# Kernel optimization log

Measured on AMD Instinct MI355X. Metric: run time of the kernel, lower is better.

The kernel has to match this reference:

```python
import jax, jax.numpy as jnp
import numpy as np
import math


def _layernorm(x, g, b, eps=1e-5):
    m = x.mean(-1, keepdims=True)
    v = x.var(-1, keepdims=True)
    return (x - m) / jnp.sqrt(v + eps) * g + b


def _ssd(log_decay, frequency, b_r, b_i, chunk):
    # SSD eigenstate evolution: chunk-local complex decay-mask matmuls + sequential inter-chunk state scan
    B, T, K = b_r.shape
    T_pad = -(-T // chunk) * chunk
    if T_pad > T:
        pad = T_pad - T
        b_r = jnp.pad(b_r, ((0, 0), (0, pad), (0, 0)))
        b_i = jnp.pad(b_i, ((0, 0), (0, pad), (0, 0)))
    n_chunks = T_pad // chunk
    mag = jax.nn.sigmoid(log_decay)                      # (K,)
    pos = jnp.arange(chunk, dtype=b_r.dtype)             # (C,)
    mag_pow = mag[None, :] ** pos[:, None]               # (C,K)
    phases = pos[:, None] * frequency[None, :]           # (C,K)
    kernel_r = mag_pow * jnp.cos(phases)
    kernel_i = mag_pow * jnp.sin(phases)
    diffs = pos[None, :] - pos[:, None]                  # (C,C), faithful to torch: pos.unsqueeze(0)-pos.unsqueeze(1)
    mask = (diffs >= 0).astype(b_r.dtype)[:, :, None]
    idx = jnp.clip(diffs, 0, None).astype(jnp.int32)
    L_r = kernel_r[idx] * mask                           # (C,C,K)
    L_i = kernel_i[idx] * mask
    Br = b_r.reshape(B, n_chunks, chunk, K)
    Bi = b_i.reshape(B, n_chunks, chunk, K)
    # intra-chunk complex contraction
    intra_r = jnp.einsum('ijk,bnjk->bnik', L_r, Br) - jnp.einsum('ijk,bnjk->bnik', L_i, Bi)
    intra_i = jnp.einsum('ijk,bnjk->bnik', L_r, Bi) + jnp.einsum('ijk,bnjk->bnik', L_i, Br)
    prop_r = L_r[:, 0, :]                                # (C,K)
    prop_i = L_i[:, 0, :]

    def step(carry, chunk_in):
        sr, si = carry                                   # (B,K)
        ir, ii = chunk_in                                # (B,C,K)
        corr_r = prop_r[None] * sr[:, None] - prop_i[None] * si[:, None]
        corr_i = prop_r[None] * si[:, None] + prop_i[None] * sr[:, None]
        out_r = ir + corr_r
        out_i = ii + corr_i
        return (out_r[:, -1], out_i[:, -1]), (out_r, out_i)

    init = (jnp.zeros((B, K), b_r.dtype), jnp.zeros((B, K), b_r.dtype))
    _, (o_r, o_i) = jax.lax.scan(step, init, (intra_r.transpose(1, 0, 2, 3), intra_i.transpose(1, 0, 2, 3)))
    c_r = o_r.transpose(1, 0, 2, 3).reshape(B, T_pad, K)[:, :T]
    c_i = o_i.transpose(1, 0, 2, 3).reshape(B, T_pad, K)[:, :T]
    return c_r, c_i


def setup_inputs() -> dict:
    B, T, D, K, H, CONV = 4, 4096, 1024, 64, 4, 4
    Kh = K // H
    mlp = 4 * D
    ks = jax.random.split(jax.random.key(0), 12)

    def n(k, shape, s):
        return (jax.random.normal(k, shape) * s).astype(jnp.float32)

    return {
        'x': n(ks[0], (B, T, D), 1.0),
        'in_proj_w': n(ks[1], (2 * K, D), 1.0 / math.sqrt(D)),
        'conv_w': n(ks[2], (2 * K, 1, CONV), 0.5),
        'conv_b': jnp.zeros((2 * K,), jnp.float32),
        'log_decay': jax.random.uniform(ks[3], (K,), minval=-3.0, maxval=-1.5).astype(jnp.float32),
        'frequency': jnp.linspace(0.0, 2 * math.pi * (1 - 1.0 / K), K).astype(jnp.float32),
        'coupling': (jnp.eye(Kh)[None] + 0.01 * jax.random.normal(ks[4], (H, Kh, Kh)) / math.sqrt(Kh)).astype(jnp.float32),
        'out_proj_w': n(ks[5], (D, 2 * K), 1.0 / math.sqrt(2 * K)),
        'gate_w': n(ks[6], (D, D), 1.0 / math.sqrt(D)),
        'gate_b': jnp.full((D,), -2.0, jnp.float32),
        'mlp_w1': n(ks[7], (mlp, D), 1.0 / math.sqrt(D)),
        'mlp_b1': jnp.zeros((mlp,), jnp.float32),
        'mlp_w2': n(ks[8], (D, mlp), 1.0 / math.sqrt(mlp)),
        'mlp_b2': jnp.zeros((D,), jnp.float32),
        'ln1_g': jnp.ones((D,), jnp.float32), 'ln1_b': jnp.zeros((D,), jnp.float32),
        'ln2_g': jnp.ones((D,), jnp.float32), 'ln2_b': jnp.zeros((D,), jnp.float32),
    }


def reference(x, in_proj_w, conv_w, conv_b, log_decay, frequency, coupling,
              out_proj_w, gate_w, gate_b, mlp_w1, mlp_b1, mlp_w2, mlp_b2,
              ln1_g, ln1_b, ln2_g, ln2_b):
    B, T, D = x.shape
    K2 = in_proj_w.shape[0]
    K = K2 // 2
    CHUNK = 64
    H, Kh = coupling.shape[0], coupling.shape[1]
    residual = x
    xn = _layernorm(x, ln1_g, ln1_b)
    beta = xn @ in_proj_w.T                              # (B,T,2K)
    kconv = conv_w.shape[-1]
    # causal depthwise conv1d (torch pads both sides then truncates to T == left-pad kconv-1)
    bc = jax.lax.conv_general_dilated(
        beta.transpose(0, 2, 1), conv_w, (1,), [(kconv - 1, 0)],
        feature_group_count=K2, dimension_numbers=('NCH', 'OIH', 'NCH'))
    beta = jax.nn.silu((bc + conv_b[None, :, None]).transpose(0, 2, 1))
    beta_r, beta_i = beta[..., :K], beta[..., K:]
    c_r, c_i = _ssd(log_decay, frequency, beta_r, beta_i, CHUNK)
    c_r = jnp.einsum('hjk,bthk->bthj', coupling, c_r.reshape(B, T, H, Kh)).reshape(B, T, K)
    c_i = jnp.einsum('hjk,bthk->bthj', coupling, c_i.reshape(B, T, H, Kh)).reshape(B, T, K)
    eig = jnp.concatenate([c_r, c_i], axis=-1)           # (B,T,2K)
    h = eig @ out_proj_w.T
    gate = jax.nn.sigmoid(xn @ gate_w.T + gate_b)
    x1 = residual + gate * h
    xn2 = _layernorm(x1, ln2_g, ln2_b)
    out = x1 + (jax.nn.silu(xn2 @ mlp_w1.T + mlp_b1) @ mlp_w2.T + mlp_b2)
    return out, eig
```

## Files before the change

kernel.cpp:

```cpp
#include <hip/hip_runtime.h>
#include <hip/hip_bf16.h>


#define FIR_LAG 20

typedef __attribute__((ext_vector_type(8))) short    bf16x8;
typedef __attribute__((ext_vector_type(4))) float    f32x4;
typedef __attribute__((ext_vector_type(4))) unsigned short ushort4_t;

__device__ __forceinline__ unsigned short f2bf(float f) {
    union { __hip_bfloat16 b; unsigned short u; } cv;
    cv.b = __float2bfloat16(f);
    return cv.u;
}
__device__ __forceinline__ float bf2f(unsigned short u) {
    return __uint_as_float((unsigned)u << 16);
}

__device__ __forceinline__ void gload_lds16(const unsigned short* g, unsigned short* l) {
    __builtin_amdgcn_global_load_lds(
        (const __attribute__((address_space(1))) unsigned int*)g,
        (__attribute__((address_space(3))) unsigned int*)l, 16, 0, 0);
}

__global__ __launch_bounds__(256) void cvt_bf16_kernel(
    const float* __restrict__ in, unsigned short* __restrict__ out, int n)
{
    int i = (blockIdx.x * 256 + threadIdx.x) * 8;
    if (i >= n) return;
    float4 a = *(const float4*)(in + i);
    float4 b = *(const float4*)(in + i + 4);
    ushort4_t o0 = { f2bf(a.x), f2bf(a.y), f2bf(a.z), f2bf(a.w) };
    ushort4_t o1 = { f2bf(b.x), f2bf(b.y), f2bf(b.z), f2bf(b.w) };
    *(ushort4_t*)(out + i)     = o0;
    *(ushort4_t*)(out + i + 4) = o1;
}

__global__ __launch_bounds__(256) void ln_kernel(
    const float* __restrict__ in, const float* __restrict__ g,
    const float* __restrict__ b, unsigned short* __restrict__ out)
{
    const size_t row = blockIdx.x;
    const int t = threadIdx.x;
    float4 v = ((const float4*)(in + row * 1024))[t];
    float s  = v.x + v.y + v.z + v.w;
    float s2 = v.x*v.x + v.y*v.y + v.z*v.z + v.w*v.w;
    #pragma unroll
    for (int o = 32; o > 0; o >>= 1) {
        s  += __shfl_down(s, o);
        s2 += __shfl_down(s2, o);
    }
    __shared__ float red[8];
    __shared__ float mv[2];
    const int wv = t >> 6;
    if ((t & 63) == 0) { red[wv] = s; red[4 + wv] = s2; }
    __syncthreads();
    if (t == 0) {
        float a  = red[0] + red[1] + red[2] + red[3];
        float a2 = red[4] + red[5] + red[6] + red[7];
        float mean = a * (1.f / 1024.f);
        float var  = a2 * (1.f / 1024.f) - mean * mean;
        mv[0] = mean;
        mv[1] = rsqrtf(var + 1e-5f);
    }
    __syncthreads();
    const float mean = mv[0], rstd = mv[1];
    float4 gg = ((const float4*)g)[t];
    float4 bb = ((const float4*)b)[t];
    ushort4_t o4 = { f2bf((v.x - mean) * rstd * gg.x + bb.x),
                     f2bf((v.y - mean) * rstd * gg.y + bb.y),
                     f2bf((v.z - mean) * rstd * gg.z + bb.z),
                     f2bf((v.w - mean) * rstd * gg.w + bb.w) };
    *(ushort4_t*)(out + row * 1024 + t * 4) = o4;
}

__global__ __launch_bounds__(256) void conv_silu_kernel(
    const float* __restrict__ bp, const float* __restrict__ cw,
    const float* __restrict__ cb, float* __restrict__ beta, int T)
{
    const int idx = blockIdx.x * 256 + threadIdx.x;
    const int c  = idx & 127;
    const int bt = idx >> 7;
    const int t  = bt & (T - 1);
    float acc = cb[c];
    #pragma unroll
    for (int j = 0; j < 4; ++j) {
        int ts = t - 3 + j;
        if (ts >= 0) acc += cw[c * 4 + j] * bp[(size_t)(bt - 3 + j) * 128 + c];
    }
    beta[(size_t)bt * 128 + c] = acc / (1.f + expf(-acc));
}

__global__ __launch_bounds__(256) void fir_coupling_kernel(
    const float* __restrict__ beta, const float* __restrict__ log_decay,
    const float* __restrict__ freq, const float* __restrict__ coup,
    float* __restrict__ eig, unsigned short* __restrict__ eig_bf, int T)
{
    __shared__ float sb[65][128];
    const int blk = blockIdx.x;
    const int nch = T >> 6;
    const int b = blk / nch;
    const int n = blk - b * nch;
    const size_t base = ((size_t)b * T + (size_t)n * 64) * 128;
    const int tid = threadIdx.x;

    #pragma unroll
    for (int it = 0; it < 8; ++it) {
        int f = tid + it * 256;
        int r = f >> 5, c4 = f & 31;
        *(float4*)&sb[1 + r][c4 * 4] =
            *(const float4*)(beta + base + (size_t)r * 128 + c4 * 4);
    }
    if (tid < 32) {
        float4 z = make_float4(0.f, 0.f, 0.f, 0.f);
        *(float4*)&sb[0][tid * 4] =
            (n > 0) ? *(const float4*)(beta + base - 128 + tid * 4) : z;
    }
    __syncthreads();

    const int k  = tid & 63;
    const int tq = tid >> 6;
    const float mag = 1.f / (1.f + expf(-log_decay[k]));
    const float w = freq[k];
    const float rr = mag * cosf(w), ri = mag * sinf(w);
    float cr[16], ci[16];
    #pragma unroll
    for (int m = 0; m < 16; ++m) { cr[m] = 0.f; ci[m] = 0.f; }
    float zr = 1.f, zi = 0.f;
    for (int e = 0; e <= FIR_LAG; ++e) {
        #pragma unroll
        for (int m = 0; m < 16; ++m) {
            int i = tq * 16 + m;
            int src = i + e;
            if (src <= 63) {
                float br = sb[1 + src][k];
                float bi = sb[1 + src][64 + k];
                cr[m] += zr * br - zi * bi;
                ci[m] += zr * bi + zi * br;
            }
        }
        float nzr = zr * rr - zi * ri;
        zi = zr * ri + zi * rr;
        zr = nzr;
    }
    if (tq == 0) {
        cr[0] += sb[0][k];
        ci[0] += sb[0][64 + k];
    }
    __syncthreads();
    #pragma unroll
    for (int m = 0; m < 16; ++m) {
        int i = tq * 16 + m;
        sb[i][k] = cr[m];
        sb[i][64 + k] = ci[m];
    }
    __syncthreads();
    const int h = k >> 4, j = k & 15;
    float cp[16];
    #pragma unroll
    for (int q = 0; q < 16; ++q) cp[q] = coup[(h * 16 + j) * 16 + q];
    #pragma unroll
    for (int m = 0; m < 16; ++m) {
        int i = tq * 16 + m;
        float sr = 0.f, si = 0.f;
        #pragma unroll
        for (int q = 0; q < 16; ++q) {
            sr += cp[q] * sb[i][h * 16 + q];
            si += cp[q] * sb[i][64 + h * 16 + q];
        }
        size_t o = base + (size_t)i * 128;
        eig[o + k]         = sr;
        eig[o + 64 + k]    = si;
        eig_bf[o + k]      = f2bf(sr);
        eig_bf[o + 64 + k] = f2bf(si);
    }
}

__global__ __launch_bounds__(256) void gemm_mfma_f32out(
    const unsigned short* __restrict__ A, const unsigned short* __restrict__ B,
    float* __restrict__ C, int M, int N, int K)
{
    constexpr int BM = 128, BK = 32;
    __shared__ unsigned short As[BM * BK];
    __shared__ unsigned short Bs[BM * BK];
    const int tid  = threadIdx.x;
    const int lane = tid & 63;
    const int wave = tid >> 6;
    const int wm = wave >> 1, wn = wave & 1;
    const int bm = blockIdx.y * BM;
    const int bn = blockIdx.x * BM;

    f32x4 acc[4][4];
    #pragma unroll
    for (int m = 0; m < 4; ++m)
        #pragma unroll
        for (int n = 0; n < 4; ++n) acc[m][n] = (f32x4){0.f, 0.f, 0.f, 0.f};

    const int frow = lane & 15;
    const int fk   = (lane >> 4) * 8;
    const int srow = tid >> 2;
    const int sc   = (tid & 3) * 8;

    for (int k0 = 0; k0 < K; k0 += BK) {
        #pragma unroll
        for (int it = 0; it < 2; ++it) {
            int row = it * 64 + srow;
            int ci  = it * 256 + tid;
            gload_lds16(A + (size_t)(bm + row) * K + k0 + sc, As + ci * 8);
            gload_lds16(B + (size_t)(bn + row) * K + k0 + sc, Bs + ci * 8);
        }
        __syncthreads();
        bf16x8 af[4], bfr[4];
        #pragma unroll
        for (int m = 0; m < 4; ++m)
            af[m] = *(const bf16x8*)(As + (wm * 64 + m * 16 + frow) * BK + fk);
        #pragma unroll
        for (int n = 0; n < 4; ++n)
            bfr[n] = *(const bf16x8*)(Bs + (wn * 64 + n * 16 + frow) * BK + fk);
        #pragma unroll
        for (int m = 0; m < 4; ++m)
            #pragma unroll
            for (int n = 0; n < 4; ++n)
                acc[m][n] = __builtin_amdgcn_mfma_f32_16x16x32_bf16(
                    af[m], bfr[n], acc[m][n], 0, 0, 0);
        __syncthreads();
    }

    const int r0 = (lane >> 4) * 4;
    const int cc = lane & 15;
    #pragma unroll
    for (int m = 0; m < 4; ++m)
        #pragma unroll
        for (int n = 0; n < 4; ++n) {
            const int col = bn + wn * 64 + n * 16 + cc;
            #pragma unroll
            for (int j = 0; j < 4; ++j) {
                const int row = bm + wm * 64 + m * 16 + r0 + j;
                C[(size_t)row * N + col] = acc[m][n][j];
            }
        }
}

template<int EPI, typename OT>
__global__ __launch_bounds__(512) void gemm256(
    const unsigned short* __restrict__ A, const unsigned short* __restrict__ B,
    OT* __restrict__ C, int M, int N, int K,
    const float* __restrict__ bias,
    const float* __restrict__ p1, const unsigned short* __restrict__ p2)
{
    constexpr int BM = 256, BN = 256;
    __shared__ unsigned short Asw[4 * 256 * 32];
    __shared__ unsigned short Bsw[4 * 256 * 32];
    const int tid  = threadIdx.x;
    const int lane = tid & 63;
    const int wave = tid >> 6;
    const int wm = wave >> 2;
    const int wn = wave & 3;

    const int nbn = N / BN;
    const int nwg = gridDim.x;
    int orig = blockIdx.x;
    int xcd = orig & 7, ixc = orig >> 3;
    int q = nwg >> 3, r = nwg & 7;
    int wgid = (xcd < r ? xcd * (q + 1) : r * (q + 1) + (xcd - r) * q) + ixc;
    const int bm = (wgid / nbn) * BM;
    const int bn = (wgid % nbn) * BN;

    f32x4 acc[8][4];
    #pragma unroll
    for (int m = 0; m < 8; ++m)
        #pragma unroll
        for (int n = 0; n < 4; ++n) acc[m][n] = (f32x4){0.f, 0.f, 0.f, 0.f};

    const int frow   = lane & 15;
    const int lk     = lane >> 4;
    const int achunk = lk ^ (frow & 3);

    const unsigned short* Abase = A + (size_t)bm * K;
    const unsigned short* Bbase = B + (size_t)bn * K;

#define STAGE_H(G, DS, KH)                                                   \
    {                                                                        \
        _Pragma("unroll")                                                    \
        for (int s = 0; s < 2; ++s) {                                        \
            int cid = s * 512 + tid;                                         \
            int row = cid >> 2, c = cid & 3;                                 \
            int gch = c ^ (row & 3);                                         \
            gload_lds16((G) + (size_t)row * K + (KH) * 32 + gch * 8,         \
                        (DS) + ((KH) & 3) * 8192 + cid * 8);                 \
        }                                                                    \
    }

#define LDA(MH, KH)                                                          \
    _Pragma("unroll")                                                        \
    for (int m = 0; m < 4; ++m) {                                            \
        int row = wm * 128 + (MH) * 64 + m * 16 + frow;                      \
        af[m] = *(const bf16x8*)(Asw + ((KH) & 3) * 8192 + row * 32 +        \
                                 achunk * 8);                                \
    }

#define LDB(KH)                                                              \
    _Pragma("unroll")                                                        \
    for (int n = 0; n < 4; ++n) {                                            \
        int row = wn * 64 + n * 16 + frow;                                   \
        bfv[n] = *(const bf16x8*)(Bsw + ((KH) & 3) * 8192 + row * 32 +       \
                                  achunk * 8);                               \
    }

#define BARRIER                                                              \
    asm volatile("s_barrier" ::: "memory");                                  \
    __builtin_amdgcn_sched_barrier(0);

#define MFMA_PH(MH)                                                          \
    asm volatile("s_waitcnt lgkmcnt(0)" ::: "memory");                       \
    __builtin_amdgcn_sched_barrier(0);                                       \
    __builtin_amdgcn_s_setprio(1);                                           \
    _Pragma("unroll")                                                        \
    for (int m = 0; m < 4; ++m)                                              \
        _Pragma("unroll")                                                    \
        for (int n = 0; n < 4; ++n)                                          \
            acc[(MH) * 4 + m][n] = __builtin_amdgcn_mfma_f32_16x16x32_bf16(  \
                af[m], bfv[n], acc[(MH) * 4 + m][n], 0, 0, 0);               \
    __builtin_amdgcn_s_setprio(0);

    const int NKH = K >> 5;

    STAGE_H(Abase, Asw, 0)
    STAGE_H(Bbase, Bsw, 0)
    STAGE_H(Abase, Asw, 1)
    STAGE_H(Bbase, Bsw, 1)
    STAGE_H(Abase, Asw, 2)
    STAGE_H(Bbase, Bsw, 2)
    asm volatile("s_waitcnt vmcnt(8)" ::: "memory");
    BARRIER

    for (int kh = 0; kh < NKH; ++kh) {
        bf16x8 af[4], bfv[4];
        LDA(0, kh)
        LDB(kh)
        if (kh + 3 < NKH) { STAGE_H(Abase, Asw, kh + 3) }
        BARRIER
        MFMA_PH(0)
        BARRIER
        LDA(1, kh)
        if (kh + 3 < NKH) { STAGE_H(Bbase, Bsw, kh + 3) }
        {
            int rem = NKH - 1 - kh;
            if (rem >= 3) {
                asm volatile("s_waitcnt vmcnt(8)" ::: "memory");
            } else if (rem == 2) {
                asm volatile("s_waitcnt vmcnt(4)" ::: "memory");
            } else if (rem == 1) {
                asm volatile("s_waitcnt vmcnt(0)" ::: "memory");
            }
        }
        BARRIER
        MFMA_PH(1)
        BARRIER
    }
#undef STAGE_H
#undef LDA
#undef LDB
#undef BARRIER
#undef MFMA_PH

    const int r0 = (lane >> 4) * 4;
    const int cc = lane & 15;
    #pragma unroll
    for (int m = 0; m < 8; ++m) {
        #pragma unroll
        for (int n = 0; n < 4; ++n) {
            const int col = bn + wn * 64 + n * 16 + cc;
            #pragma unroll
            for (int j = 0; j < 4; ++j) {
                const int row = bm + wm * 128 + m * 16 + r0 + j;
                const size_t idx = (size_t)row * N + col;
                const float v = acc[m][n][j];
                if constexpr (EPI == 0) {
                    C[idx] = v;
                } else if constexpr (EPI == 1) {
                    float pre = v + bias[col];
                    float gt = 1.f / (1.f + expf(-pre));
                    C[idx] = p1[idx] + gt * bf2f(p2[idx]);
                } else if constexpr (EPI == 2) {
                    float pre = v + bias[col];
                    C[idx] = (OT)__float2bfloat16(pre / (1.f + expf(-pre)));
                } else if constexpr (EPI == 3) {
                    C[idx] = p1[idx] + v + bias[col];
                } else {
                    C[idx] = (OT)__float2bfloat16(v);
                }
            }
        }
    }
}

extern "C" void kernel_launch(void* const* d_in, const int* in_sizes, int n_in,
                              void* d_out, int out_size, void* d_ws, size_t ws_size,
                              hipStream_t stream)
{
    const float* x        = (const float*)d_in[0];
    const float* in_proj  = (const float*)d_in[1];
    const float* conv_w   = (const float*)d_in[2];
    const float* conv_b   = (const float*)d_in[3];
    const float* log_dec  = (const float*)d_in[4];
    const float* freq     = (const float*)d_in[5];
    const float* coup     = (const float*)d_in[6];
    const float* out_proj = (const float*)d_in[7];
    const float* gate_w   = (const float*)d_in[8];
    const float* gate_b   = (const float*)d_in[9];
    const float* mlp_w1   = (const float*)d_in[10];
    const float* mlp_b1   = (const float*)d_in[11];
    const float* mlp_w2   = (const float*)d_in[12];
    const float* mlp_b2   = (const float*)d_in[13];
    const float* ln1_g    = (const float*)d_in[14];
    const float* ln1_b    = (const float*)d_in[15];
    const float* ln2_g    = (const float*)d_in[16];
    const float* ln2_b    = (const float*)d_in[17];

    const int B = 4, T = 4096, D = 1024;
    const int M = B * T;

    float* out = (float*)d_out;
    float* eig = out + (size_t)M * D;
    float* bpre = eig;

    char* w = (char*)d_ws;
    unsigned short* xn_bf = (unsigned short*)w; w += (size_t)M * 1024 * 2;
    float* x1             = (float*)w;          w += (size_t)M * 1024 * 4;
    float* beta           = (float*)w;          w += (size_t)M * 128 * 4;
    unsigned short* mid   = (unsigned short*)w; w += (size_t)M * 4096 * 2;
    unsigned short* eig_bf= (unsigned short*)w; w += (size_t)M * 128 * 2;
    unsigned short* wb_inproj = (unsigned short*)w; w += (size_t)128 * 1024 * 2;
    unsigned short* wb_outproj= (unsigned short*)w; w += (size_t)1024 * 128 * 2;
    unsigned short* wb_gate   = (unsigned short*)w; w += (size_t)1024 * 1024 * 2;
    unsigned short* wb_mlp1   = (unsigned short*)w; w += (size_t)4096 * 1024 * 2;
    unsigned short* wb_mlp2   = (unsigned short*)w; w += (size_t)1024 * 4096 * 2;
    unsigned short* h_bf = mid;

    cvt_bf16_kernel<<<(128 * 1024) / 2048, 256, 0, stream>>>(in_proj, wb_inproj, 128 * 1024);
    cvt_bf16_kernel<<<(1024 * 128) / 2048, 256, 0, stream>>>(out_proj, wb_outproj, 1024 * 128);
    cvt_bf16_kernel<<<(1024 * 1024) / 2048, 256, 0, stream>>>(gate_w, wb_gate, 1024 * 1024);
    cvt_bf16_kernel<<<(4096 * 1024) / 2048, 256, 0, stream>>>(mlp_w1, wb_mlp1, 4096 * 1024);
    cvt_bf16_kernel<<<(1024 * 4096) / 2048, 256, 0, stream>>>(mlp_w2, wb_mlp2, 1024 * 4096);

    ln_kernel<<<M, 256, 0, stream>>>(x, ln1_g, ln1_b, xn_bf);
    gemm_mfma_f32out<<<dim3(1, M / 128), 256, 0, stream>>>(
        xn_bf, wb_inproj, bpre, M, 128, 1024);
    conv_silu_kernel<<<(M * 128) / 256, 256, 0, stream>>>(bpre, conv_w, conv_b, beta, T);
    fir_coupling_kernel<<<B * (T / 64), 256, 0, stream>>>(
        beta, log_dec, freq, coup, eig, eig_bf, T);
    gemm256<4, __hip_bfloat16><<<(M / 256) * (1024 / 256), 512, 0, stream>>>(
        eig_bf, wb_outproj, (__hip_bfloat16*)h_bf, M, 1024, 128,
        nullptr, nullptr, nullptr);
    gemm256<1, float><<<(M / 256) * (1024 / 256), 512, 0, stream>>>(
        xn_bf, wb_gate, x1, M, 1024, 1024, gate_b, x, h_bf);
    ln_kernel<<<M, 256, 0, stream>>>(x1, ln2_g, ln2_b, xn_bf);
    gemm256<2, __hip_bfloat16><<<(M / 256) * (4096 / 256), 512, 0, stream>>>(
        xn_bf, wb_mlp1, (__hip_bfloat16*)mid, M, 4096, 1024, mlp_b1, nullptr, nullptr);
    gemm256<3, float><<<(M / 256) * (1024 / 256), 512, 0, stream>>>(
        mid, wb_mlp2, out, M, 1024, 4096, mlp_b2, x1, nullptr);
}
```

Before: 563.5 us.

## Double-buffer BK=64 tiles with 8-chunk XOR swizzle in gemm256

Replaces the four-slot ring of 32-wide K half-tiles (prefetched three ahead) with two buffers of 64-wide K tiles, each split into two 32-wide halves. It also adopts a row-pair layout whose 8 chunks are XOR-swizzled by row pair. The aim is to cut LDS bank conflicts and the number of vmcnt waits and barriers per unit of K. The trade-off is a shallower prefetch distance, which may expose more global-load latency.

```diff
diff --git a/kernel.cpp b/kernel.cpp
--- a/kernel.cpp
+++ b/kernel.cpp
@@ -248,9 +248,9 @@
     const float* __restrict__ bias,
     const float* __restrict__ p1, const unsigned short* __restrict__ p2)
 {
-    constexpr int BM = 256, BN = 256;
-    __shared__ unsigned short Asw[4 * 256 * 32];
-    __shared__ unsigned short Bsw[4 * 256 * 32];
+    constexpr int BM = 256, BN = 256, BK = 64;
+    __shared__ unsigned short As[2 * 2 * 8192];
+    __shared__ unsigned short Bs[2 * 2 * 8192];
     const int tid  = threadIdx.x;
     const int lane = tid & 63;
     const int wave = tid >> 6;
@@ -272,46 +272,47 @@
         #pragma unroll
         for (int n = 0; n < 4; ++n) acc[m][n] = (f32x4){0.f, 0.f, 0.f, 0.f};
 
-    const int frow   = lane & 15;
-    const int lk     = lane >> 4;
-    const int achunk = lk ^ (frow & 3);
+    const int frow = lane & 15;
+    const int lk   = lane >> 4;
 
     const unsigned short* Abase = A + (size_t)bm * K;
     const unsigned short* Bbase = B + (size_t)bn * K;
 
-#define STAGE_H(G, DS, KH)                                                   \
+#define STAGE(G, LB, NBUF, KH, K0)                                           \
     {                                                                        \
         _Pragma("unroll")                                                    \
         for (int s = 0; s < 2; ++s) {                                        \
             int cid = s * 512 + tid;                                         \
-            int row = cid >> 2, c = cid & 3;                                 \
-            int gch = c ^ (row & 3);                                         \
-            gload_lds16((G) + (size_t)row * K + (KH) * 32 + gch * 8,         \
-                        (DS) + ((KH) & 3) * 8192 + cid * 8);                 \
+            int rp  = cid >> 3, cp = cid & 7;                                \
+            int c   = cp ^ (rp & 7);                                         \
+            int g   = 2 * rp + (c >> 2);                                     \
+            gload_lds16((G) + (size_t)g * K + (K0) + (KH) * 32 + (c & 3) * 8,\
+                        (LB) + ((NBUF) * 2 + (KH)) * 8192 + cid * 8);        \
         }                                                                    \
     }
 
-#define LDA(MH, KH)                                                          \
+#define LDA(MH, KH, BUF)                                                     \
     _Pragma("unroll")                                                        \
     for (int m = 0; m < 4; ++m) {                                            \
-        int row = wm * 128 + (MH) * 64 + m * 16 + frow;                      \
-        af[m] = *(const bf16x8*)(Asw + ((KH) & 3) * 8192 + row * 32 +        \
-                                 achunk * 8);                                \
-    }
-
-#define LDB(KH)                                                              \
+        int R  = wm * 128 + (MH) * 64 + m * 16 + frow;                       \
+        int rp = R >> 1;                                                     \
+        int ch = (((R & 1) << 2) | lk) ^ (rp & 7);                           \
+        af[m] = *(const bf16x8*)(As + ((BUF) * 2 + (KH)) * 8192 +            \
+                                 rp * 64 + ch * 8);                          \
+    }
+
+#define LDB(KH, BUF)                                                         \
     _Pragma("unroll")                                                        \
     for (int n = 0; n < 4; ++n) {                                            \
-        int row = wn * 64 + n * 16 + frow;                                   \
-        bfv[n] = *(const bf16x8*)(Bsw + ((KH) & 3) * 8192 + row * 32 +       \
-                                  achunk * 8);                               \
-    }
-
-#define BARRIER                                                              \
+        int R  = wn * 64 + n * 16 + frow;                                    \
+        int rp = R >> 1;                                                     \
+        int ch = (((R & 1) << 2) | lk) ^ (rp & 7);                           \
+        bfv[n] = *(const bf16x8*)(Bs + ((BUF) * 2 + (KH)) * 8192 +           \
+                                  rp * 64 + ch * 8);                         \
+    }
+
+#define PH_TAIL(MH)                                                          \
     asm volatile("s_barrier" ::: "memory");                                  \
-    __builtin_amdgcn_sched_barrier(0);
-
-#define MFMA_PH(MH)                                                          \
     asm volatile("s_waitcnt lgkmcnt(0)" ::: "memory");                       \
     __builtin_amdgcn_sched_barrier(0);                                       \
     __builtin_amdgcn_s_setprio(1);                                           \
@@ -321,48 +322,48 @@
         for (int n = 0; n < 4; ++n)                                          \
             acc[(MH) * 4 + m][n] = __builtin_amdgcn_mfma_f32_16x16x32_bf16(  \
                 af[m], bfv[n], acc[(MH) * 4 + m][n], 0, 0, 0);               \
-    __builtin_amdgcn_s_setprio(0);
-
-    const int NKH = K >> 5;
-
-    STAGE_H(Abase, Asw, 0)
-    STAGE_H(Bbase, Bsw, 0)
-    STAGE_H(Abase, Asw, 1)
-    STAGE_H(Bbase, Bsw, 1)
-    STAGE_H(Abase, Asw, 2)
-    STAGE_H(Bbase, Bsw, 2)
-    asm volatile("s_waitcnt vmcnt(8)" ::: "memory");
-    BARRIER
-
-    for (int kh = 0; kh < NKH; ++kh) {
+    __builtin_amdgcn_s_setprio(0);                                           \
+    __builtin_amdgcn_sched_barrier(0);
+
+#define VM4 asm volatile("s_waitcnt vmcnt(4)" ::: "memory");
+#define VM0 asm volatile("s_waitcnt vmcnt(0)" ::: "memory");
+
+    const int NT = K / BK;
+
+    STAGE(Abase, As, 0, 0, 0)
+    STAGE(Bbase, Bs, 0, 0, 0)
+    STAGE(Abase, As, 0, 1, 0)
+    STAGE(Bbase, Bs, 0, 1, 0)
+    VM4
+    asm volatile("s_barrier" ::: "memory");
+
+    for (int t = 0; t < NT; ++t) {
+        const int buf = t & 1, nbuf = buf ^ 1;
+        const int kn = (t + 1) * BK;
+        const bool pre = (t + 1 < NT);
         bf16x8 af[4], bfv[4];
-        LDA(0, kh)
-        LDB(kh)
-        if (kh + 3 < NKH) { STAGE_H(Abase, Asw, kh + 3) }
-        BARRIER
-        MFMA_PH(0)
-        BARRIER
-        LDA(1, kh)
-        if (kh + 3 < NKH) { STAGE_H(Bbase, Bsw, kh + 3) }
-        {
-            int rem = NKH - 1 - kh;
-            if (rem >= 3) {
-                asm volatile("s_waitcnt vmcnt(8)" ::: "memory");
-            } else if (rem == 2) {
-                asm volatile("s_waitcnt vmcnt(4)" ::: "memory");
-            } else if (rem == 1) {
-                asm volatile("s_waitcnt vmcnt(0)" ::: "memory");
-            }
-        }
-        BARRIER
-        MFMA_PH(1)
-        BARRIER
-    }
-#undef STAGE_H
+
+        LDA(0, 0, buf)
+        LDB(0, buf)
+        if (pre) { STAGE(Abase, As, nbuf, 0, kn) }
+        PH_TAIL(0)
+        LDA(1, 0, buf)
+        if (pre) { STAGE(Bbase, Bs, nbuf, 0, kn) VM4 } else { VM0 }
+        PH_TAIL(1)
+        LDA(0, 1, buf)
+        LDB(1, buf)
+        if (pre) { STAGE(Abase, As, nbuf, 1, kn) }
+        PH_TAIL(0)
+        LDA(1, 1, buf)
+        if (pre) { STAGE(Bbase, Bs, nbuf, 1, kn) VM4 }
+        PH_TAIL(1)
+    }
+#undef STAGE
 #undef LDA
 #undef LDB
-#undef BARRIER
-#undef MFMA_PH
+#undef PH_TAIL
+#undef VM4
+#undef VM0
 
     const int r0 = (lane >> 4) * 4;
     const int cc = lane & 15;
@@ -379,12 +380,12 @@
                 if constexpr (EPI == 0) {
                     C[idx] = v;
                 } else if constexpr (EPI == 1) {
-                    float pre = v + bias[col];
-                    float gt = 1.f / (1.f + expf(-pre));
+                    float pre_ = v + bias[col];
+                    float gt = 1.f / (1.f + expf(-pre_));
                     C[idx] = p1[idx] + gt * bf2f(p2[idx]);
                 } else if constexpr (EPI == 2) {
-                    float pre = v + bias[col];
-                    C[idx] = (OT)__float2bfloat16(pre / (1.f + expf(-pre)));
+                    float pre_ = v + bias[col];
+                    C[idx] = (OT)__float2bfloat16(pre_ / (1.f + expf(-pre_)));
                 } else if constexpr (EPI == 3) {
                     C[idx] = p1[idx] + v + bias[col];
                 } else {
```

After: 549.0 us. 1.03x faster.
